# Kernel optimization log

Measured on AMD Instinct MI355X. Metric: run time of the kernel, lower is better.

## Reference

```python
import jax, jax.numpy as jnp
import numpy as np

BLOCK = 128          # quantization block size (K-blocks for activations, 128x128 for weight)
FP8_MAX = 448.0      # max normal of float8_e4m3fn


def _quant_weight(w):
    """Block-quantize a [N, K] weight to fp8 values (stored in f32) + [N/128, K/128] scales."""
    N, K = w.shape
    wb = w.reshape(N // BLOCK, BLOCK, K // BLOCK, BLOCK)
    ws = jnp.max(jnp.abs(wb), axis=(1, 3)) / FP8_MAX          # [N/128, K/128]
    ws_full = jnp.repeat(jnp.repeat(ws, BLOCK, axis=0), BLOCK, axis=1)  # [N, K]
    w_fp8 = (w / ws_full).astype(jnp.float8_e4m3fn).astype(jnp.float32)
    return w_fp8, ws


def setup_inputs() -> dict:
    key = jax.random.key(0)
    k1, k2 = jax.random.split(key)
    x = jax.random.normal(k1, (4, 2048, 4096), dtype=jnp.float32)
    w = jax.random.normal(k2, (4096, 4096), dtype=jnp.float32) * 0.02
    weight, weight_scale = _quant_weight(w)
    return {"x": x, "weight": weight, "weight_scale": weight_scale}


def reference(x, weight, weight_scale):
    """FP8Linear forward: dynamic per-128-block activation quant + scaled fp8 GEMM.

    x:            [..., K] float32
    weight:       [N, K]   fp8 values stored as float32
    weight_scale: [N/128, K/128] float32 per-block weight scales
    """
    *lead, K = x.shape
    N = weight.shape[0]
    # --- act_quant: per-row, per-128-K-block dynamic scale, round-trip through fp8 ---
    xb = x.reshape(-1, K // BLOCK, BLOCK)                      # [M, Kb, 128]
    s = jnp.max(jnp.abs(xb), axis=-1, keepdims=True) / FP8_MAX # [M, Kb, 1]
    xq = (xb / s).astype(jnp.float8_e4m3fn).astype(jnp.float32)
    a = (xq * s).reshape(-1, K)                                # dequantized activations [M, K]
    # --- fp8_gemm: per-block dequant folds into the accumulation; since scales are
    # constant within each K-block, this equals a plain GEMM of dequantized operands ---
    ws_full = jnp.repeat(jnp.repeat(weight_scale, BLOCK, axis=0), BLOCK, axis=1)  # [N, K]
    w_deq = weight * ws_full
    y = a @ w_deq.T                                            # [M, N] fp32 accumulate
    return y.reshape(*lead, N)
```

## Files before the change

kernel.cpp:

```cpp
#include <hip/hip_runtime.h>
#include <hip/hip_fp8.h>
#include <stdint.h>

#define K_DIM 4096
#define N_DIM 4096
#define NKB   32

using f32x4 = __attribute__((ext_vector_type(4))) float;
using i32x4 = __attribute__((ext_vector_type(4))) int;
using i32x8 = __attribute__((ext_vector_type(8))) int;

#define GLOAD_LDS16(g, l)                                                      \
    __builtin_amdgcn_global_load_lds(                                          \
        (const __attribute__((address_space(1))) unsigned int*)(g),            \
        (__attribute__((address_space(3))) unsigned int*)(l), 16, 0, 0)

__device__ __forceinline__ uint8_t to_fp8(float v) {
    __hip_fp8_e4m3 q(v);
    return (uint8_t)q.__x;
}

__global__ __launch_bounds__(256) void act_quant_kernel(
    const float* __restrict__ x, uint8_t* __restrict__ xq,
    float* __restrict__ sa)
{
    int gw   = blockIdx.x * 4 + (threadIdx.x >> 6);
    int lane = threadIdx.x & 63;
    int m    = gw >> 5;
    int kb   = gw & 31;
    size_t base = (size_t)m * K_DIM + kb * 128 + lane * 2;
    float2 v = *(const float2*)(x + base);
    float amax = fmaxf(fabsf(v.x), fabsf(v.y));
    #pragma unroll
    for (int o = 32; o >= 1; o >>= 1) amax = fmaxf(amax, __shfl_xor(amax, o));
    float s = amax / 448.0f;
    uchar2 q;
    q.x = to_fp8(v.x / s);
    q.y = to_fp8(v.y / s);
    *(uchar2*)(xq + base) = q;
    if (lane == 0) sa[(size_t)m * NKB + kb] = s;
}

__global__ __launch_bounds__(256) void w_quant_kernel(
    const float* __restrict__ w, uint8_t* __restrict__ wq)
{
    size_t i = ((size_t)blockIdx.x * 256 + threadIdx.x) * 4;
    float4 v = *(const float4*)(w + i);
    uchar4 q;
    q.x = to_fp8(v.x); q.y = to_fp8(v.y); q.z = to_fp8(v.z); q.w = to_fp8(v.w);
    *(uchar4*)(wq + i) = q;
}

__global__ __launch_bounds__(256) void fp8_gemm_mx(
    const uint8_t* __restrict__ Aq, const uint8_t* __restrict__ Bq,
    const float* __restrict__ sa, const float* __restrict__ wscale,
    float* __restrict__ C, int mTiles)
{
    __shared__ __align__(16) uint8_t lA[128 * 128];
    __shared__ __align__(16) uint8_t lB[128 * 128];
    __shared__ float lS[128];

    const int t    = threadIdx.x;
    const int lane = t & 63;
    const int wid  = t >> 6;
    const int lr   = lane & 15;
    const int lk   = lane >> 4;
    const int wr   = (wid >> 1) * 64;
    const int wc   = (wid & 1) * 64;

    const int nTiles = N_DIM / 128;
    int nwg = mTiles * nTiles;
    int cpx = nwg >> 3;
    int bid = blockIdx.x;
    int swz = (bid & 7) * cpx + (bid >> 3);
    int mT = swz / nTiles, nT = swz % nTiles;
    const int m0 = mT * 128, n0 = nT * 128;

    const int srow = t >> 3;
    const int lcol = ((t & 7) ^ (srow & 7)) * 16;
    const uint8_t* gA = Aq + (size_t)(m0 + srow) * K_DIM + lcol;
    const uint8_t* gB = Bq + (size_t)(n0 + srow) * K_DIM + lcol;
    const int ldst = t * 16;

    const int fswz = (lr & 7) << 4;
    const int c0 = (lk * 32) ^ fswz;
    const int c1 = (lk * 32 + 16) ^ fswz;

    f32x4 acc[4][4] = {};
    const f32x4 vzero = {0.f, 0.f, 0.f, 0.f};

    for (int kb = 0; kb < NKB; ++kb) {
        size_t ko = (size_t)kb * 128;
        #pragma unroll
        for (int i = 0; i < 4; ++i) {
            GLOAD_LDS16(gA + ko + (size_t)i * 32 * K_DIM, &lA[i * 4096 + ldst]);
            GLOAD_LDS16(gB + ko + (size_t)i * 32 * K_DIM, &lB[i * 4096 + ldst]);
        }
        if (t < 128)
            lS[t] = sa[(size_t)(m0 + t) * NKB + kb] * wscale[nT * NKB + kb];
        __syncthreads();

        i32x8 af[4], bf[4];
        #pragma unroll
        for (int mi = 0; mi < 4; ++mi) {
            int ab = (wr + mi * 16 + lr) * 128;
            i32x4 lo = *(const i32x4*)&lA[ab + c0];
            i32x4 hi = *(const i32x4*)&lA[ab + c1];
            af[mi][0] = lo[0]; af[mi][1] = lo[1]; af[mi][2] = lo[2]; af[mi][3] = lo[3];
            af[mi][4] = hi[0]; af[mi][5] = hi[1]; af[mi][6] = hi[2]; af[mi][7] = hi[3];
        }
        #pragma unroll
        for (int ni = 0; ni < 4; ++ni) {
            int bb = (wc + ni * 16 + lr) * 128;
            i32x4 lo = *(const i32x4*)&lB[bb + c0];
            i32x4 hi = *(const i32x4*)&lB[bb + c1];
            bf[ni][0] = lo[0]; bf[ni][1] = lo[1]; bf[ni][2] = lo[2]; bf[ni][3] = lo[3];
            bf[ni][4] = hi[0]; bf[ni][5] = hi[1]; bf[ni][6] = hi[2]; bf[ni][7] = hi[3];
        }

        #pragma unroll
        for (int mi = 0; mi < 4; ++mi) {
            f32x4 s4 = *(const f32x4*)&lS[wr + mi * 16 + lk * 4];
            f32x4 bs[4];
            #pragma unroll
            for (int ni = 0; ni < 4; ++ni)
                bs[ni] = __builtin_amdgcn_mfma_scale_f32_16x16x128_f8f6f4(
                    af[mi], bf[ni], vzero, 0, 0,
                    0, 0x7F7F7F7F, 0, 0x7F7F7F7F);
            #pragma unroll
            for (int ni = 0; ni < 4; ++ni)
                acc[mi][ni] += bs[ni] * s4;
        }
        __syncthreads();
    }

    #pragma unroll
    for (int mi = 0; mi < 4; ++mi) {
        #pragma unroll
        for (int j = 0; j < 4; ++j) {
            int m = m0 + wr + mi * 16 + lk * 4 + j;
            float* crow = C + (size_t)m * N_DIM + n0 + wc;
            #pragma unroll
            for (int ni = 0; ni < 4; ++ni)
                crow[ni * 16 + lr] = acc[mi][ni][j];
        }
    }
}

extern "C" void kernel_launch(void* const* d_in, const int* in_sizes, int n_in,
                              void* d_out, int out_size, void* d_ws, size_t ws_size,
                              hipStream_t stream) {
    const float* x      = (const float*)d_in[0];
    const float* w      = (const float*)d_in[1];
    const float* wscale = (const float*)d_in[2];
    float* out = (float*)d_out;
    int M = in_sizes[0] / K_DIM;

    uint8_t* xq = (uint8_t*)d_ws;
    uint8_t* wq = xq + (size_t)M * K_DIM;
    float*   sa = (float*)(wq + (size_t)N_DIM * K_DIM);

    act_quant_kernel<<<M * NKB / 4, 256, 0, stream>>>(x, xq, sa);
    w_quant_kernel<<<((size_t)N_DIM * K_DIM) / 1024, 256, 0, stream>>>(w, wq);

    int mTiles = M / 128;
    fp8_gemm_mx<<<mTiles * (N_DIM / 128), 256, 0, stream>>>(
        xq, wq, sa, wscale, out, mTiles);
}
```

Before: 289.4 us.

## Double-buffer 256x256 fp8 GEMM tiles with prefetch and transposed activation scales

```diff
diff --git a/kernel.cpp b/kernel.cpp
--- a/kernel.cpp
+++ b/kernel.cpp
@@ -14,6 +14,10 @@
     __builtin_amdgcn_global_load_lds(                                          \
         (const __attribute__((address_space(1))) unsigned int*)(g),            \
         (__attribute__((address_space(3))) unsigned int*)(l), 16, 0, 0)
+#define GLOAD_LDS4(g, l)                                                       \
+    __builtin_amdgcn_global_load_lds(                                          \
+        (const __attribute__((address_space(1))) unsigned int*)(g),            \
+        (__attribute__((address_space(3))) unsigned int*)(l), 4, 0, 0)
 
 __device__ __forceinline__ uint8_t to_fp8(float v) {
     __hip_fp8_e4m3 q(v);
@@ -22,7 +26,7 @@
 
 __global__ __launch_bounds__(256) void act_quant_kernel(
     const float* __restrict__ x, uint8_t* __restrict__ xq,
-    float* __restrict__ sa)
+    float* __restrict__ saT, int M)
 {
     int gw   = blockIdx.x * 4 + (threadIdx.x >> 6);
     int lane = threadIdx.x & 63;
@@ -38,7 +42,7 @@
     q.x = to_fp8(v.x / s);
     q.y = to_fp8(v.y / s);
     *(uchar2*)(xq + base) = q;
-    if (lane == 0) sa[(size_t)m * NKB + kb] = s;
+    if (lane == 0) saT[(size_t)kb * M + m] = s;
 }
 
 __global__ __launch_bounds__(256) void w_quant_kernel(
@@ -51,98 +55,145 @@
     *(uchar4*)(wq + i) = q;
 }
 
-__global__ __launch_bounds__(256) void fp8_gemm_mx(
+#define LS_A(b) ((b) * 65536)
+#define LS_B(b) ((b) * 65536 + 32768)
+#define LS_S(b) (131072 + (b) * 1024)
+
+__global__ __launch_bounds__(512, 2) void fp8_gemm_mx2(
     const uint8_t* __restrict__ Aq, const uint8_t* __restrict__ Bq,
-    const float* __restrict__ sa, const float* __restrict__ wscale,
-    float* __restrict__ C, int mTiles)
+    const float* __restrict__ saT, const float* __restrict__ wscale,
+    float* __restrict__ C, int M)
 {
-    __shared__ __align__(16) uint8_t lA[128 * 128];
-    __shared__ __align__(16) uint8_t lB[128 * 128];
-    __shared__ float lS[128];
+    __shared__ __align__(16) uint8_t lds[133120];
 
     const int t    = threadIdx.x;
     const int lane = t & 63;
-    const int wid  = t >> 6;
     const int lr   = lane & 15;
     const int lk   = lane >> 4;
-    const int wr   = (wid >> 1) * 64;
-    const int wc   = (wid & 1) * 64;
-
-    const int nTiles = N_DIM / 128;
-    int nwg = mTiles * nTiles;
+    const int wid  = t >> 6;
+    const int wm   = wid >> 2;
+    const int wn   = wid & 3;
+
+    const int gridN = N_DIM / 256;
+    int nwg = (M / 256) * gridN;
     int cpx = nwg >> 3;
     int bid = blockIdx.x;
     int swz = (bid & 7) * cpx + (bid >> 3);
-    int mT = swz / nTiles, nT = swz % nTiles;
-    const int m0 = mT * 128, n0 = nT * 128;
+    const int m0 = (swz / gridN) * 256;
+    const int n0 = (swz % gridN) * 256;
+    const int nbI = ((n0 >> 7) + (wn >> 1)) * NKB;
 
     const int srow = t >> 3;
-    const int lcol = ((t & 7) ^ (srow & 7)) * 16;
-    const uint8_t* gA = Aq + (size_t)(m0 + srow) * K_DIM + lcol;
-    const uint8_t* gB = Bq + (size_t)(n0 + srow) * K_DIM + lcol;
-    const int ldst = t * 16;
-
-    const int fswz = (lr & 7) << 4;
-    const int c0 = (lk * 32) ^ fswz;
-    const int c1 = (lk * 32 + 16) ^ fswz;
-
-    f32x4 acc[4][4] = {};
+    const int scol = ((t & 7) ^ (srow & 7)) * 16;
+    const uint8_t* gA = Aq + (size_t)(m0 + srow) * K_DIM + scol;
+    const uint8_t* gB = Bq + (size_t)(n0 + srow) * K_DIM + scol;
+    const int dst = t * 16;
+
+    const int fsw = (lr & 7) << 4;
+
+    f32x4 acc[8][4] = {};
     const f32x4 vzero = {0.f, 0.f, 0.f, 0.f};
 
-    for (int kb = 0; kb < NKB; ++kb) {
-        size_t ko = (size_t)kb * 128;
+    #pragma unroll
+    for (int j = 0; j < 4; ++j) {
+        GLOAD_LDS16(gA + (size_t)j * 64 * K_DIM, &lds[LS_A(0) + j * 8192 + dst]);
+        GLOAD_LDS16(gB + (size_t)j * 64 * K_DIM, &lds[LS_B(0) + j * 8192 + dst]);
+    }
+    if (wid < 4)
+        GLOAD_LDS4(saT + m0 + wid * 64 + lane,
+                   &lds[LS_S(0) + wid * 256 + lane * 4]);
+    asm volatile("s_waitcnt vmcnt(0)" ::: "memory");
+    __builtin_amdgcn_s_barrier();
+
+    for (int i = 0; i < 32; ++i) {
+        const int cur = i & 1;
+        const int nxt = cur ^ 1;
+        const int kbn = (i + 1) & 31;
+        const int aB = LS_A(cur);
+        const int bB = LS_B(cur);
+        const int sB = LS_S(cur);
+        const float rw = wscale[nbI + i];
+
         #pragma unroll
-        for (int i = 0; i < 4; ++i) {
-            GLOAD_LDS16(gA + ko + (size_t)i * 32 * K_DIM, &lA[i * 4096 + ldst]);
-            GLOAD_LDS16(gB + ko + (size_t)i * 32 * K_DIM, &lB[i * 4096 + ldst]);
+        for (int ph = 0; ph < 4; ++ph) {
+            const int mh = ph >> 1, nh = ph & 1;
+
+            i32x8 af[4], bfr[2];
+            #pragma unroll
+            for (int mi = 0; mi < 4; ++mi) {
+                int rb = (wm * 128 + mh * 64 + mi * 16 + lr) * 128;
+                int c0 = (lk * 32) ^ fsw;
+                i32x4 lo = *(const i32x4*)&lds[aB + rb + c0];
+                i32x4 hi = *(const i32x4*)&lds[aB + rb + (c0 ^ 16)];
+                af[mi][0] = lo[0]; af[mi][1] = lo[1]; af[mi][2] = lo[2]; af[mi][3] = lo[3];
+                af[mi][4] = hi[0]; af[mi][5] = hi[1]; af[mi][6] = hi[2]; af[mi][7] = hi[3];
+            }
+            #pragma unroll
+            for (int ni = 0; ni < 2; ++ni) {
+                int rb = (wn * 64 + nh * 32 + ni * 16 + lr) * 128;
+                int c0 = (lk * 32) ^ fsw;
+                i32x4 lo = *(const i32x4*)&lds[bB + rb + c0];
+                i32x4 hi = *(const i32x4*)&lds[bB + rb + (c0 ^ 16)];
+                bfr[ni][0] = lo[0]; bfr[ni][1] = lo[1]; bfr[ni][2] = lo[2]; bfr[ni][3] = lo[3];
+                bfr[ni][4] = hi[0]; bfr[ni][5] = hi[1]; bfr[ni][6] = hi[2]; bfr[ni][7] = hi[3];
+            }
+
+            if (ph == 0) {
+                #pragma unroll
+                for (int j = 0; j < 4; ++j)
+                    GLOAD_LDS16(gA + (size_t)kbn * 128 + (size_t)j * 64 * K_DIM,
+                                &lds[LS_A(nxt) + j * 8192 + dst]);
+            }
+            if (ph == 1) {
+                #pragma unroll
+                for (int j = 0; j < 4; ++j)
+                    GLOAD_LDS16(gB + (size_t)kbn * 128 + (size_t)j * 64 * K_DIM,
+                                &lds[LS_B(nxt) + j * 8192 + dst]);
+                if (wid < 4)
+                    GLOAD_LDS4(saT + (size_t)kbn * M + m0 + wid * 64 + lane,
+                               &lds[LS_S(nxt) + wid * 256 + lane * 4]);
+            }
+
+            __builtin_amdgcn_s_barrier();
+            asm volatile("s_waitcnt lgkmcnt(0)" ::: "memory");
+            __builtin_amdgcn_sched_barrier(0);
+
+            f32x4 bs[4][2];
+            __builtin_amdgcn_s_setprio(1);
+            #pragma unroll
+            for (int mi = 0; mi < 4; ++mi)
+                #pragma unroll
+                for (int ni = 0; ni < 2; ++ni)
+                    bs[mi][ni] = __builtin_amdgcn_mfma_scale_f32_16x16x128_f8f6f4(
+                        af[mi], bfr[ni], vzero, 0, 0,
+                        0, 0x7F7F7F7F, 0, 0x7F7F7F7F);
+            __builtin_amdgcn_s_setprio(0);
+
+            #pragma unroll
+            for (int mi = 0; mi < 4; ++mi) {
+                f32x4 s4 = *(const f32x4*)&lds[sB + (wm * 128 + mh * 64 + mi * 16 + lk * 4) * 4];
+                f32x4 sc = s4 * rw;
+                acc[mh * 4 + mi][nh * 2 + 0] += bs[mi][0] * sc;
+                acc[mh * 4 + mi][nh * 2 + 1] += bs[mi][1] * sc;
+            }
+
+            if (ph == 3) asm volatile("s_waitcnt vmcnt(0)" ::: "memory");
+            __builtin_amdgcn_s_barrier();
         }
-        if (t < 128)
-            lS[t] = sa[(size_t)(m0 + t) * NKB + kb] * wscale[nT * NKB + kb];
-        __syncthreads();
-
-        i32x8 af[4], bf[4];
-        #pragma unroll
-        for (int mi = 0; mi < 4; ++mi) {
-            int ab = (wr + mi * 16 + lr) * 128;
-            i32x4 lo = *(const i32x4*)&lA[ab + c0];
-            i32x4 hi = *(const i32x4*)&lA[ab + c1];
-            af[mi][0] = lo[0]; af[mi][1] = lo[1]; af[mi][2] = lo[2]; af[mi][3] = lo[3];
-            af[mi][4] = hi[0]; af[mi][5] = hi[1]; af[mi][6] = hi[2]; af[mi][7] = hi[3];
-        }
-        #pragma unroll
-        for (int ni = 0; ni < 4; ++ni) {
-            int bb = (wc + ni * 16 + lr) * 128;
-            i32x4 lo = *(const i32x4*)&lB[bb + c0];
-            i32x4 hi = *(const i32x4*)&lB[bb + c1];
-            bf[ni][0] = lo[0]; bf[ni][1] = lo[1]; bf[ni][2] = lo[2]; bf[ni][3] = lo[3];
-            bf[ni][4] = hi[0]; bf[ni][5] = hi[1]; bf[ni][6] = hi[2]; bf[ni][7] = hi[3];
-        }
-
-        #pragma unroll
-        for (int mi = 0; mi < 4; ++mi) {
-            f32x4 s4 = *(const f32x4*)&lS[wr + mi * 16 + lk * 4];
-            f32x4 bs[4];
-            #pragma unroll
-            for (int ni = 0; ni < 4; ++ni)
-                bs[ni] = __builtin_amdgcn_mfma_scale_f32_16x16x128_f8f6f4(
-                    af[mi], bf[ni], vzero, 0, 0,
-                    0, 0x7F7F7F7F, 0, 0x7F7F7F7F);
-            #pragma unroll
-            for (int ni = 0; ni < 4; ++ni)
-                acc[mi][ni] += bs[ni] * s4;
-        }
-        __syncthreads();
     }
 
     #pragma unroll
-    for (int mi = 0; mi < 4; ++mi) {
+    for (int q = 0; q < 8; ++q) {
+        int mh = q >> 2, mi = q & 3;
         #pragma unroll
         for (int j = 0; j < 4; ++j) {
-            int m = m0 + wr + mi * 16 + lk * 4 + j;
-            float* crow = C + (size_t)m * N_DIM + n0 + wc;
-            #pragma unroll
-            for (int ni = 0; ni < 4; ++ni)
-                crow[ni * 16 + lr] = acc[mi][ni][j];
+            int m = m0 + wm * 128 + mh * 64 + mi * 16 + lk * 4 + j;
+            float* crow = C + (size_t)m * N_DIM + n0 + wn * 64;
+            #pragma unroll
+            for (int nc = 0; nc < 4; ++nc) {
+                int nh = nc >> 1, ni = nc & 1;
+                crow[nh * 32 + ni * 16 + lr] = acc[q][nc][j];
+            }
         }
     }
 }
@@ -156,14 +207,13 @@
     float* out = (float*)d_out;
     int M = in_sizes[0] / K_DIM;
 
-    uint8_t* xq = (uint8_t*)d_ws;
-    uint8_t* wq = xq + (size_t)M * K_DIM;
-    float*   sa = (float*)(wq + (size_t)N_DIM * K_DIM);
-
-    act_quant_kernel<<<M * NKB / 4, 256, 0, stream>>>(x, xq, sa);
+    uint8_t* xq  = (uint8_t*)d_ws;
+    uint8_t* wq  = xq + (size_t)M * K_DIM;
+    float*   saT = (float*)(wq + (size_t)N_DIM * K_DIM);
+
+    act_quant_kernel<<<M * NKB / 4, 256, 0, stream>>>(x, xq, saT, M);
     w_quant_kernel<<<((size_t)N_DIM * K_DIM) / 1024, 256, 0, stream>>>(w, wq);
 
-    int mTiles = M / 128;
-    fp8_gemm_mx<<<mTiles * (N_DIM / 128), 256, 0, stream>>>(
-        xq, wq, sa, wscale, out, mTiles);
-}
+    int nwg = (M / 256) * (N_DIM / 256);
+    fp8_gemm_mx2<<<nwg, 512, 0, stream>>>(xq, wq, saT, wscale, out, M);
+}
```

New measurement: 400.2 us. +38.3%, slower.

## Double-buffer LDS tiles and prefetch transposed activation scales in FP8 GEMM

Applied to the files above, without the earlier changes.

```diff
diff --git a/kernel.cpp b/kernel.cpp
--- a/kernel.cpp
+++ b/kernel.cpp
@@ -14,6 +14,10 @@
     __builtin_amdgcn_global_load_lds(                                          \
         (const __attribute__((address_space(1))) unsigned int*)(g),            \
         (__attribute__((address_space(3))) unsigned int*)(l), 16, 0, 0)
+#define GLOAD_LDS4(g, l)                                                       \
+    __builtin_amdgcn_global_load_lds(                                          \
+        (const __attribute__((address_space(1))) unsigned int*)(g),            \
+        (__attribute__((address_space(3))) unsigned int*)(l), 4, 0, 0)
 
 __device__ __forceinline__ uint8_t to_fp8(float v) {
     __hip_fp8_e4m3 q(v);
@@ -22,7 +26,7 @@
 
 __global__ __launch_bounds__(256) void act_quant_kernel(
     const float* __restrict__ x, uint8_t* __restrict__ xq,
-    float* __restrict__ sa)
+    float* __restrict__ saT, int M)
 {
     int gw   = blockIdx.x * 4 + (threadIdx.x >> 6);
     int lane = threadIdx.x & 63;
@@ -38,7 +42,7 @@
     q.x = to_fp8(v.x / s);
     q.y = to_fp8(v.y / s);
     *(uchar2*)(xq + base) = q;
-    if (lane == 0) sa[(size_t)m * NKB + kb] = s;
+    if (lane == 0) saT[(size_t)kb * M + m] = s;
 }
 
 __global__ __launch_bounds__(256) void w_quant_kernel(
@@ -51,14 +55,16 @@
     *(uchar4*)(wq + i) = q;
 }
 
-__global__ __launch_bounds__(256) void fp8_gemm_mx(
+#define LSA(b) ((b) * 33280)
+#define LSB(b) ((b) * 33280 + 16384)
+#define LSS(b) ((b) * 33280 + 32768)
+
+__global__ __launch_bounds__(256, 2) void fp8_gemm_mx3(
     const uint8_t* __restrict__ Aq, const uint8_t* __restrict__ Bq,
-    const float* __restrict__ sa, const float* __restrict__ wscale,
-    float* __restrict__ C, int mTiles)
+    const float* __restrict__ saT, const float* __restrict__ wscale,
+    float* __restrict__ C, int M)
 {
-    __shared__ __align__(16) uint8_t lA[128 * 128];
-    __shared__ __align__(16) uint8_t lB[128 * 128];
-    __shared__ float lS[128];
+    __shared__ __align__(16) uint8_t lds[66560];
 
     const int t    = threadIdx.x;
     const int lane = t & 63;
@@ -69,6 +75,7 @@
     const int wc   = (wid & 1) * 64;
 
     const int nTiles = N_DIM / 128;
+    int mTiles = M / 128;
     int nwg = mTiles * nTiles;
     int cpx = nwg >> 3;
     int bid = blockIdx.x;
@@ -77,50 +84,62 @@
     const int m0 = mT * 128, n0 = nT * 128;
 
     const int srow = t >> 3;
-    const int lcol = ((t & 7) ^ (srow & 7)) * 16;
-    const uint8_t* gA = Aq + (size_t)(m0 + srow) * K_DIM + lcol;
-    const uint8_t* gB = Bq + (size_t)(n0 + srow) * K_DIM + lcol;
+    const int scol = ((t & 7) ^ (srow & 7)) * 16;
+    const uint8_t* gA = Aq + (size_t)(m0 + srow) * K_DIM + scol;
+    const uint8_t* gB = Bq + (size_t)(n0 + srow) * K_DIM + scol;
     const int ldst = t * 16;
 
-    const int fswz = (lr & 7) << 4;
-    const int c0 = (lk * 32) ^ fswz;
-    const int c1 = (lk * 32 + 16) ^ fswz;
+    const int fsw = (lr & 7) << 4;
+    const int c0  = (lk * 32) ^ fsw;
+
+#define STAGE(buf, kbi) do {                                                   \
+    size_t ko_ = (size_t)(kbi) * 128;                                          \
+    _Pragma("unroll") for (int j = 0; j < 4; ++j) {                            \
+        GLOAD_LDS16(gA + ko_ + (size_t)j * 32 * K_DIM,                         \
+                    &lds[LSA(buf) + j * 4096 + ldst]);                         \
+        GLOAD_LDS16(gB + ko_ + (size_t)j * 32 * K_DIM,                         \
+                    &lds[LSB(buf) + j * 4096 + ldst]);                         \
+    }                                                                          \
+    if (wid < 2)                                                               \
+        GLOAD_LDS4(saT + (size_t)(kbi) * M + m0 + wid * 64 + lane,             \
+                   &lds[LSS(buf) + wid * 256 + lane * 4]);                     \
+} while (0)
 
     f32x4 acc[4][4] = {};
     const f32x4 vzero = {0.f, 0.f, 0.f, 0.f};
 
+    STAGE(0, 0);
+    asm volatile("s_waitcnt vmcnt(0)" ::: "memory");
+    __builtin_amdgcn_s_barrier();
+
+    #pragma unroll 2
     for (int kb = 0; kb < NKB; ++kb) {
-        size_t ko = (size_t)kb * 128;
-        #pragma unroll
-        for (int i = 0; i < 4; ++i) {
-            GLOAD_LDS16(gA + ko + (size_t)i * 32 * K_DIM, &lA[i * 4096 + ldst]);
-            GLOAD_LDS16(gB + ko + (size_t)i * 32 * K_DIM, &lB[i * 4096 + ldst]);
-        }
-        if (t < 128)
-            lS[t] = sa[(size_t)(m0 + t) * NKB + kb] * wscale[nT * NKB + kb];
-        __syncthreads();
+        const int cur = kb & 1;
+        if (kb < NKB - 1) STAGE(cur ^ 1, kb + 1);
+
+        const int aB = LSA(cur), bB = LSB(cur), sB = LSS(cur);
+        const float rw = wscale[nT * NKB + kb];
 
         i32x8 af[4], bf[4];
         #pragma unroll
         for (int mi = 0; mi < 4; ++mi) {
-            int ab = (wr + mi * 16 + lr) * 128;
-            i32x4 lo = *(const i32x4*)&lA[ab + c0];
-            i32x4 hi = *(const i32x4*)&lA[ab + c1];
-            af[mi][0] = lo[0]; af[mi][1] = lo[1]; af[mi][2] = lo[2]; af[mi][3] = lo[3];
-            af[mi][4] = hi[0]; af[mi][5] = hi[1]; af[mi][6] = hi[2]; af[mi][7] = hi[3];
+            int rb = aB + (wr + mi * 16 + lr) * 128;
+            i32x4 lo = *(const i32x4*)&lds[rb + c0];
+            i32x4 hi = *(const i32x4*)&lds[rb + (c0 ^ 16)];
+            af[mi] = __builtin_shufflevector(lo, hi, 0, 1, 2, 3, 4, 5, 6, 7);
         }
         #pragma unroll
         for (int ni = 0; ni < 4; ++ni) {
-            int bb = (wc + ni * 16 + lr) * 128;
-            i32x4 lo = *(const i32x4*)&lB[bb + c0];
-            i32x4 hi = *(const i32x4*)&lB[bb + c1];
-            bf[ni][0] = lo[0]; bf[ni][1] = lo[1]; bf[ni][2] = lo[2]; bf[ni][3] = lo[3];
-            bf[ni][4] = hi[0]; bf[ni][5] = hi[1]; bf[ni][6] = hi[2]; bf[ni][7] = hi[3];
+            int rb = bB + (wc + ni * 16 + lr) * 128;
+            i32x4 lo = *(const i32x4*)&lds[rb + c0];
+            i32x4 hi = *(const i32x4*)&lds[rb + (c0 ^ 16)];
+            bf[ni] = __builtin_shufflevector(lo, hi, 0, 1, 2, 3, 4, 5, 6, 7);
         }
 
         #pragma unroll
         for (int mi = 0; mi < 4; ++mi) {
-            f32x4 s4 = *(const f32x4*)&lS[wr + mi * 16 + lk * 4];
+            f32x4 s4 = *(const f32x4*)&lds[sB + (wr + mi * 16 + lk * 4) * 4];
+            f32x4 sc = s4 * rw;
             f32x4 bs[4];
             #pragma unroll
             for (int ni = 0; ni < 4; ++ni)
@@ -129,10 +148,13 @@
                     0, 0x7F7F7F7F, 0, 0x7F7F7F7F);
             #pragma unroll
             for (int ni = 0; ni < 4; ++ni)
-                acc[mi][ni] += bs[ni] * s4;
+                acc[mi][ni] += bs[ni] * sc;
         }
-        __syncthreads();
+
+        asm volatile("s_waitcnt vmcnt(0)" ::: "memory");
+        __builtin_amdgcn_s_barrier();
     }
+#undef STAGE
 
     #pragma unroll
     for (int mi = 0; mi < 4; ++mi) {
@@ -156,14 +178,13 @@
     float* out = (float*)d_out;
     int M = in_sizes[0] / K_DIM;
 
-    uint8_t* xq = (uint8_t*)d_ws;
-    uint8_t* wq = xq + (size_t)M * K_DIM;
-    float*   sa = (float*)(wq + (size_t)N_DIM * K_DIM);
+    uint8_t* xq  = (uint8_t*)d_ws;
+    uint8_t* wq  = xq + (size_t)M * K_DIM;
+    float*   saT = (float*)(wq + (size_t)N_DIM * K_DIM);
 
-    act_quant_kernel<<<M * NKB / 4, 256, 0, stream>>>(x, xq, sa);
+    act_quant_kernel<<<M * NKB / 4, 256, 0, stream>>>(x, xq, saT, M);
     w_quant_kernel<<<((size_t)N_DIM * K_DIM) / 1024, 256, 0, stream>>>(w, wq);
 
-    int mTiles = M / 128;
-    fp8_gemm_mx<<<mTiles * (N_DIM / 128), 256, 0, stream>>>(
-        xq, wq, sa, wscale, out, mTiles);
+    int nwg = (M / 128) * (N_DIM / 128);
+    fp8_gemm_mx3<<<nwg, 256, 0, stream>>>(xq, wq, saT, wscale, out, M);
 }
```

Measured after the change: 262.8 us. 1.1x faster.
